# Performance work log

Hardware: AMD Instinct MI355X
Metric: run time of the kernel (lower is better)

The kernel has to match this reference:

```python
import jax, jax.numpy as jnp
import numpy as np

IMG_H, IMG_W = 800, 800
OUT_H, OUT_W = 7, 7
SR = 2  # sampling_ratio (exact sampling branch)
SCALES = (0.25, 0.125, 0.0625, 0.03125)
CANONICAL_SCALE = 224.0
CANONICAL_LEVEL = 4.0
K_MIN, K_MAX = 2, 5  # -log2(0.25), -log2(1/32)
EPS = 1e-6


def _prep_coords(c, size):
    # c: continuous coords (K, N); returns low/high int indices and lerp weights
    c = jnp.maximum(c, 0.0)
    lo = c.astype(jnp.int32)  # truncation == floor for c >= 0
    at_edge = lo >= size - 1
    hi = jnp.where(at_edge, size - 1, lo + 1)
    lo = jnp.where(at_edge, size - 1, lo)
    l = c - lo.astype(c.dtype)
    return lo, hi, l, 1.0 - l


def roi_align_exact(feat, batch_idx, rois, scale):
    # feat: (B, C, H, W); batch_idx: (K,) int; rois: (K, 4) xyxy; exact sampling, aligned=False
    B, C, H, W = feat.shape
    x1 = rois[:, 0] * scale
    y1 = rois[:, 1] * scale
    x2 = rois[:, 2] * scale
    y2 = rois[:, 3] * scale
    roi_w = jnp.maximum(x2 - x1, 1.0)
    roi_h = jnp.maximum(y2 - y1, 1.0)
    bin_h = roi_h / OUT_H
    bin_w = roi_w / OUT_W
    ph = jnp.arange(OUT_H, dtype=feat.dtype)
    pw = jnp.arange(OUT_W, dtype=feat.dtype)
    iy = jnp.arange(SR, dtype=feat.dtype)
    ix = jnp.arange(SR, dtype=feat.dtype)
    # (K, OUT_H, SR) -> (K, OUT_H*SR)
    y = y1[:, None, None] + ph[None, :, None] * bin_h[:, None, None] + (iy[None, None, :] + 0.5) * (bin_h / SR)[:, None, None]
    x = x1[:, None, None] + pw[None, :, None] * bin_w[:, None, None] + (ix[None, None, :] + 0.5) * (bin_w / SR)[:, None, None]
    K = rois.shape[0]
    NY, NX = OUT_H * SR, OUT_W * SR
    y = y.reshape(K, NY)
    x = x.reshape(K, NX)
    y_lo, y_hi, ly, hy = _prep_coords(y, H)
    x_lo, x_hi, lx, hx = _prep_coords(x, W)

    b = batch_idx[:, None, None]

    def gather(yi, xi):
        # -> (K, NY, NX, C): advanced indices around ':' put (K,NY,NX) in front
        return feat[b, :, yi[:, :, None], xi[:, None, :]]

    val = (hy[:, :, None, None] * hx[:, None, :, None] * gather(y_lo, x_lo)
           + hy[:, :, None, None] * lx[:, None, :, None] * gather(y_lo, x_hi)
           + ly[:, :, None, None] * hx[:, None, :, None] * gather(y_hi, x_lo)
           + ly[:, :, None, None] * lx[:, None, :, None] * gather(y_hi, x_hi))
    # (K, OUT_H, SR, OUT_W, SR, C) -> sum sampling grid, avg by count
    val = val.reshape(K, OUT_H, SR, OUT_W, SR, C).sum(axis=(2, 4)) / float(SR * SR)
    return jnp.transpose(val, (0, 3, 1, 2))  # (K, C, OUT_H, OUT_W)


def multiscale_roi_align(feats, boxes):
    B, L, _ = boxes.shape
    K = B * L
    rois = boxes.reshape(K, 4)
    batch_idx = jnp.repeat(jnp.arange(B, dtype=jnp.int32), L)
    area = (rois[:, 2] - rois[:, 0]) * (rois[:, 3] - rois[:, 1])
    s = jnp.sqrt(area)
    lvl = jnp.floor(CANONICAL_LEVEL + jnp.log2(s / CANONICAL_SCALE) + EPS)
    levels = jnp.clip(lvl, K_MIN, K_MAX).astype(jnp.int32) - K_MIN
    C = feats[0].shape[1]
    out = jnp.zeros((K, C, OUT_H, OUT_W), dtype=feats[0].dtype)
    for l, (f, sc) in enumerate(zip(feats, SCALES)):
        pooled = roi_align_exact(f, batch_idx, rois, sc)
        out = out + jnp.where((levels == l)[:, None, None, None], pooled, 0.0)
    return out


def setup_inputs() -> dict:
    key = jax.random.key(0)
    k0, k1, k2, k3, kw, kh, kx, ky = jax.random.split(key, 8)
    B, C, L = 2, 256, 256
    feat0 = jax.random.normal(k0, (B, C, 200, 200), dtype=jnp.float32)
    feat1 = jax.random.normal(k1, (B, C, 100, 100), dtype=jnp.float32)
    feat2 = jax.random.normal(k2, (B, C, 50, 50), dtype=jnp.float32)
    feat3 = jax.random.normal(k3, (B, C, 25, 25), dtype=jnp.float32)
    w = jax.random.uniform(kw, (B, L), minval=16.0, maxval=512.0)
    h = jax.random.uniform(kh, (B, L), minval=16.0, maxval=512.0)
    x1 = jax.random.uniform(kx, (B, L)) * (IMG_W - w)
    y1 = jax.random.uniform(ky, (B, L)) * (IMG_H - h)
    boxes = jnp.stack([x1, y1, x1 + w, y1 + h], axis=-1).astype(jnp.float32)
    return {"feat0": feat0, "feat1": feat1, "feat2": feat2, "feat3": feat3, "boxes": boxes}


def reference(feat0, feat1, feat2, feat3, boxes):
    return multiscale_roi_align([feat0, feat1, feat2, feat3], boxes)
```

## Files before the change

kernel.cpp:

```cpp
#include <hip/hip_runtime.h>


#define OUT_HW 7
#define NCH 256
#define CC 8
#define PM 1152
#define WSTRIDE 80
#define NROI 512
#define THREADS 512


__device__ __forceinline__ void roi_scalars(const float* __restrict__ boxes, int k,
    int& lvl, int& H, int& W, float& x1, float& y1, float& bin_w, float& bin_h,
    int& px0, int& py0, int& pw_cnt, int& ph_cnt)
{
    float bx1 = boxes[k*4+0], by1 = boxes[k*4+1], bx2 = boxes[k*4+2], by2 = boxes[k*4+3];
    float area = (bx2-bx1)*(by2-by1);
    float s = sqrtf(area);
    float lvlf = floorf(4.0f + log2f(s*(1.0f/224.0f)) + 1e-6f);
    lvlf = fminf(fmaxf(lvlf, 2.0f), 5.0f);
    lvl = (int)lvlf - 2;
    float scale;
    if (lvl == 0)      { H=200; W=200; scale=0.25f;    }
    else if (lvl == 1) { H=100; W=100; scale=0.125f;   }
    else if (lvl == 2) { H=50;  W=50;  scale=0.0625f;  }
    else               { H=25;  W=25;  scale=0.03125f; }
    x1 = bx1*scale; y1 = by1*scale;
    float roi_w = fmaxf(bx2*scale - x1, 1.0f);
    float roi_h = fmaxf(by2*scale - y1, 1.0f);
    bin_w = roi_w*(1.0f/7.0f); bin_h = roi_h*(1.0f/7.0f);
    float c; int lo;
    c = fmaxf(x1 + 0.25f*bin_w, 0.0f); lo = (int)c; px0 = (lo >= W-1) ? (W-1) : lo;
    c = fmaxf(x1 + 6.75f*bin_w, 0.0f); lo = (int)c; int px1e = (lo >= W-1) ? (W-1) : (lo+1);
    c = fmaxf(y1 + 0.25f*bin_h, 0.0f); lo = (int)c; py0 = (lo >= H-1) ? (H-1) : lo;
    c = fmaxf(y1 + 6.75f*bin_h, 0.0f); lo = (int)c; int py1e = (lo >= H-1) ? (H-1) : (lo+1);
    pw_cnt = px1e - px0 + 1;
    ph_cnt = py1e - py0 + 1;
}

__global__ __launch_bounds__(64) void roi_setup(const float* __restrict__ boxes,
                                                int* __restrict__ ws)
{
    int k = blockIdx.x*64 + threadIdx.x;
    if (k >= NROI) return;
    int lvl, H, W, px0, py0, pw_cnt, ph_cnt;
    float x1, y1, bin_w, bin_h;
    roi_scalars(boxes, k, lvl, H, W, x1, y1, bin_w, bin_h, px0, py0, pw_cnt, ph_cnt);
    int pw_pad = (pw_cnt + 1) | 1;
    int* p = ws + k*WSTRIDE;
    p[0]=lvl; p[1]=px0; p[2]=py0; p[3]=pw_cnt; p[4]=pw_pad;
    p[5]=pw_cnt*ph_cnt; p[6]=W; p[7]=H*W; p[8]=ph_cnt;
    for (int i = 0; i < 14; ++i) {
        float c = fmaxf(x1 + ((float)i*0.5f + 0.25f)*bin_w, 0.0f);
        int lo = (int)c; int xle; float lx;
        if (lo >= W-1) { xle = (W-1) - px0; lx = 0.0f; }
        else           { xle = lo - px0;    lx = c - (float)lo; }
        p[16+i] = xle;
        p[30+i] = __float_as_int(lx);
    }
    for (int i = 0; i < 14; ++i) {
        float c = fmaxf(y1 + ((float)i*0.5f + 0.25f)*bin_h, 0.0f);
        int lo = (int)c; int r; float ly;
        if (lo >= H-1) { r = (H-1) - py0; ly = 0.0f; }
        else           { r = lo - py0;    ly = c - (float)lo; }
        p[44+i] = r*pw_pad;
        p[58+i] = __float_as_int(ly);
    }
}

template<bool USE_WS>
__global__ __launch_bounds__(THREADS) void msroi_main(
    const float* __restrict__ f0, const float* __restrict__ f1,
    const float* __restrict__ f2, const float* __restrict__ f3,
    const float* __restrict__ boxes, const int* __restrict__ ws,
    float* __restrict__ out)
{
    __shared__ float s_patch[CC*PM];
    __shared__ int   s_taps[56];

    const int tid = threadIdx.x;
    const int k  = blockIdx.y;
    const int c0 = blockIdx.x * CC;

    int lvl, px0, py0, pw_cnt, pw_pad, pdense, W, HW, ph_cnt;
    if constexpr (USE_WS) {
        const int* p = ws + k*WSTRIDE;
        lvl = p[0]; px0 = p[1]; py0 = p[2]; pw_cnt = p[3]; pw_pad = p[4];
        pdense = p[5]; W = p[6]; HW = p[7]; ph_cnt = p[8];
        if (tid < 56) s_taps[tid] = p[16 + tid];
    } else {
        int H; float x1, y1, bin_w, bin_h;
        roi_scalars(boxes, k, lvl, H, W, x1, y1, bin_w, bin_h, px0, py0, pw_cnt, ph_cnt);
        pw_pad = (pw_cnt + 1) | 1; pdense = pw_cnt*ph_cnt; HW = H*W;
        if (tid < 14) {
            float c = fmaxf(x1 + ((float)tid*0.5f + 0.25f)*bin_w, 0.0f);
            int lo = (int)c; int xle; float lx;
            if (lo >= W-1) { xle = (W-1) - px0; lx = 0.0f; }
            else           { xle = lo - px0;    lx = c - (float)lo; }
            s_taps[tid] = xle; s_taps[14+tid] = __float_as_int(lx);
        } else if (tid >= 64 && tid < 78) {
            int i = tid - 64;
            float c = fmaxf(y1 + ((float)i*0.5f + 0.25f)*bin_h, 0.0f);
            int lo = (int)c; int r; float ly;
            if (lo >= H-1) { r = (H-1) - py0; ly = 0.0f; }
            else           { r = lo - py0;    ly = c - (float)lo; }
            s_taps[28+i] = r*pw_pad; s_taps[42+i] = __float_as_int(ly);
        }
    }

    const float* feat = (lvl == 0) ? f0 : (lvl == 1) ? f1 : (lvl == 2) ? f2 : f3;
    const int b = k >> 8;
    const float* bp = feat + (size_t)(b*NCH + c0) * (size_t)HW;

    int nz = ph_cnt + 1 + pw_cnt;
    for (int z = tid; z < nz; z += THREADS) {
        int wi = (z <= ph_cnt) ? (z*pw_pad + pw_cnt)
                               : (ph_cnt*pw_pad + (z - (ph_cnt + 1)));
#pragma unroll
        for (int j = 0; j < CC; ++j) s_patch[j*PM + wi] = 0.0f;
    }

    float inv_pw = 1.0f / (float)pw_cnt;
    for (int i = tid; i < pdense; i += THREADS) {
        int r = (int)((float)i * inv_pw);
        int col = i - r*pw_cnt;
        if (col < 0)             { col += pw_cnt; --r; }
        else if (col >= pw_cnt)  { col -= pw_cnt; ++r; }
        int go = (py0 + r)*W + (px0 + col);
        int wi = r*pw_pad + col;
#pragma unroll
        for (int j = 0; j < CC; ++j)
            s_patch[j*PM + wi] = bp[(size_t)j*(size_t)HW + (size_t)go];
    }
    __syncthreads();

    if (tid < CC*49) {
        int cl = tid / 49, pix = tid - cl*49;
        int ph = pix / 7,  pw  = pix - ph*7;
        int cb = cl*PM;
        int xl0 = s_taps[2*pw]   + cb;
        int xl1 = s_taps[2*pw+1] + cb;
        float lx0 = __int_as_float(s_taps[14 + 2*pw]);
        float lx1 = __int_as_float(s_taps[15 + 2*pw]);
        int r00 = s_taps[28 + 2*ph];
        int r01 = s_taps[29 + 2*ph];
        float ly0 = __int_as_float(s_taps[42 + 2*ph]);
        float ly1 = __int_as_float(s_taps[43 + 2*ph]);
        float hx0 = 1.0f - lx0, hx1 = 1.0f - lx1;
        float hy0 = 1.0f - ly0, hy1 = 1.0f - ly1;

        float acc = 0.0f;
        {
            int a = r00 + xl0, a2 = a + pw_pad;
            float v00 = s_patch[a], v01 = s_patch[a+1];
            float v10 = s_patch[a2], v11 = s_patch[a2+1];
            acc += hy0*(hx0*v00 + lx0*v01) + ly0*(hx0*v10 + lx0*v11);
        }
        {
            int a = r00 + xl1, a2 = a + pw_pad;
            float v00 = s_patch[a], v01 = s_patch[a+1];
            float v10 = s_patch[a2], v11 = s_patch[a2+1];
            acc += hy0*(hx1*v00 + lx1*v01) + ly0*(hx1*v10 + lx1*v11);
        }
        {
            int a = r01 + xl0, a2 = a + pw_pad;
            float v00 = s_patch[a], v01 = s_patch[a+1];
            float v10 = s_patch[a2], v11 = s_patch[a2+1];
            acc += hy1*(hx0*v00 + lx0*v01) + ly1*(hx0*v10 + lx0*v11);
        }
        {
            int a = r01 + xl1, a2 = a + pw_pad;
            float v00 = s_patch[a], v01 = s_patch[a+1];
            float v10 = s_patch[a2], v11 = s_patch[a2+1];
            acc += hy1*(hx1*v00 + lx1*v01) + ly1*(hx1*v10 + lx1*v11);
        }
        out[((size_t)k*NCH + c0)*49 + tid] = acc * 0.25f;
    }
}

extern "C" void kernel_launch(void* const* d_in, const int* in_sizes, int n_in,
                              void* d_out, int out_size, void* d_ws, size_t ws_size,
                              hipStream_t stream)
{
    const float* f0 = (const float*)d_in[0];
    const float* f1 = (const float*)d_in[1];
    const float* f2 = (const float*)d_in[2];
    const float* f3 = (const float*)d_in[3];
    const float* boxes = (const float*)d_in[4];
    float* out = (float*)d_out;

    dim3 grid(NCH / CC, NROI, 1);
    dim3 block(THREADS, 1, 1);
    size_t need = (size_t)NROI * WSTRIDE * sizeof(int);

    if (d_ws != nullptr && ws_size >= need) {
        roi_setup<<<dim3((NROI + 63)/64), dim3(64), 0, stream>>>(boxes, (int*)d_ws);
        msroi_main<true><<<grid, block, 0, stream>>>(f0, f1, f2, f3, boxes,
                                                     (const int*)d_ws, out);
    } else {
        msroi_main<false><<<grid, block, 0, stream>>>(f0, f1, f2, f3, boxes,
                                                      nullptr, out);
    }
}
```

Baseline: 176.9 us.

## Double-buffer channel chunks via direct global-to-LDS loads per block

Each block now processes 64 channels in 8 chunks of 8. It double-buffers the staged patch in LDS, loading the next chunk with global_load_lds while the current one is interpolated. The padded patch layout is replaced by a dense pw_cnt stride with a zeroed tail, and tap offsets are read once into registers. This cuts grid size and per-block setup and overlaps load with compute, but it lowers the number of blocks and so the parallelism, and it depends on async-copy wait semantics.

```diff
diff --git a/kernel.cpp b/kernel.cpp
--- a/kernel.cpp
+++ b/kernel.cpp
@@ -1,13 +1,18 @@
 #include <hip/hip_runtime.h>
 
 
-#define OUT_HW 7
 #define NCH 256
 #define CC 8
-#define PM 1152
+#define CHUNKS 8
+#define CPB (CC * CHUNKS)
+#define PM 1153
 #define WSTRIDE 80
 #define NROI 512
 #define THREADS 512
+#define NPIX (CC * 49)
+
+typedef const __attribute__((address_space(1))) void* gas_ptr;
+typedef __attribute__((address_space(3))) void* las_ptr;
 
 
 __device__ __forceinline__ void roi_scalars(const float* __restrict__ boxes, int k,
@@ -46,10 +51,10 @@
     int lvl, H, W, px0, py0, pw_cnt, ph_cnt;
     float x1, y1, bin_w, bin_h;
     roi_scalars(boxes, k, lvl, H, W, x1, y1, bin_w, bin_h, px0, py0, pw_cnt, ph_cnt);
-    int pw_pad = (pw_cnt + 1) | 1;
+    int pdense = pw_cnt * ph_cnt;
     int* p = ws + k*WSTRIDE;
-    p[0]=lvl; p[1]=px0; p[2]=py0; p[3]=pw_cnt; p[4]=pw_pad;
-    p[5]=pw_cnt*ph_cnt; p[6]=W; p[7]=H*W; p[8]=ph_cnt;
+    p[0]=lvl; p[1]=px0; p[2]=py0; p[3]=pw_cnt; p[4]=pdense; p[5]=W; p[6]=H*W;
+    p[7]=(pdense + THREADS - 1)/THREADS;
     for (int i = 0; i < 14; ++i) {
         float c = fmaxf(x1 + ((float)i*0.5f + 0.25f)*bin_w, 0.0f);
         int lo = (int)c; int xle; float lx;
@@ -63,118 +68,141 @@
         int lo = (int)c; int r; float ly;
         if (lo >= H-1) { r = (H-1) - py0; ly = 0.0f; }
         else           { r = lo - py0;    ly = c - (float)lo; }
-        p[44+i] = r*pw_pad;
+        p[44+i] = r*pw_cnt;
         p[58+i] = __float_as_int(ly);
     }
 }
 
 template<bool USE_WS>
-__global__ __launch_bounds__(THREADS) void msroi_main(
+__global__ __launch_bounds__(THREADS) void msroi_pipe(
     const float* __restrict__ f0, const float* __restrict__ f1,
     const float* __restrict__ f2, const float* __restrict__ f3,
     const float* __restrict__ boxes, const int* __restrict__ ws,
     float* __restrict__ out)
 {
-    __shared__ float s_patch[CC*PM];
-    __shared__ int   s_taps[56];
+    __shared__ float s_patch[2][CC * PM];
 
     const int tid = threadIdx.x;
     const int k  = blockIdx.y;
-    const int c0 = blockIdx.x * CC;
-
-    int lvl, px0, py0, pw_cnt, pw_pad, pdense, W, HW, ph_cnt;
+    const int c0 = blockIdx.x * CPB;
+
+    int lvl, px0, py0, pw_cnt, pdense, W, HW, nit;
+    int Hf = 0; float x1f = 0, y1f = 0, bwf = 0, bhf = 0;
     if constexpr (USE_WS) {
         const int* p = ws + k*WSTRIDE;
-        lvl = p[0]; px0 = p[1]; py0 = p[2]; pw_cnt = p[3]; pw_pad = p[4];
-        pdense = p[5]; W = p[6]; HW = p[7]; ph_cnt = p[8];
-        if (tid < 56) s_taps[tid] = p[16 + tid];
+        lvl = p[0]; px0 = p[1]; py0 = p[2]; pw_cnt = p[3];
+        pdense = p[4]; W = p[5]; HW = p[6]; nit = p[7];
     } else {
-        int H; float x1, y1, bin_w, bin_h;
-        roi_scalars(boxes, k, lvl, H, W, x1, y1, bin_w, bin_h, px0, py0, pw_cnt, ph_cnt);
-        pw_pad = (pw_cnt + 1) | 1; pdense = pw_cnt*ph_cnt; HW = H*W;
-        if (tid < 14) {
-            float c = fmaxf(x1 + ((float)tid*0.5f + 0.25f)*bin_w, 0.0f);
-            int lo = (int)c; int xle; float lx;
-            if (lo >= W-1) { xle = (W-1) - px0; lx = 0.0f; }
-            else           { xle = lo - px0;    lx = c - (float)lo; }
-            s_taps[tid] = xle; s_taps[14+tid] = __float_as_int(lx);
-        } else if (tid >= 64 && tid < 78) {
-            int i = tid - 64;
-            float c = fmaxf(y1 + ((float)i*0.5f + 0.25f)*bin_h, 0.0f);
-            int lo = (int)c; int r; float ly;
-            if (lo >= H-1) { r = (H-1) - py0; ly = 0.0f; }
-            else           { r = lo - py0;    ly = c - (float)lo; }
-            s_taps[28+i] = r*pw_pad; s_taps[42+i] = __float_as_int(ly);
-        }
+        int ph_cnt;
+        roi_scalars(boxes, k, lvl, Hf, W, x1f, y1f, bwf, bhf, px0, py0, pw_cnt, ph_cnt);
+        pdense = pw_cnt * ph_cnt; HW = Hf * W;
+        nit = (pdense + THREADS - 1)/THREADS;
     }
 
     const float* feat = (lvl == 0) ? f0 : (lvl == 1) ? f1 : (lvl == 2) ? f2 : f3;
     const int b = k >> 8;
     const float* bp = feat + (size_t)(b*NCH + c0) * (size_t)HW;
 
-    int nz = ph_cnt + 1 + pw_cnt;
-    for (int z = tid; z < nz; z += THREADS) {
-        int wi = (z <= ph_cnt) ? (z*pw_pad + pw_cnt)
-                               : (ph_cnt*pw_pad + (z - (ph_cnt + 1)));
-#pragma unroll
-        for (int j = 0; j < CC; ++j) s_patch[j*PM + wi] = 0.0f;
-    }
-
-    float inv_pw = 1.0f / (float)pw_cnt;
-    for (int i = tid; i < pdense; i += THREADS) {
-        int r = (int)((float)i * inv_pw);
-        int col = i - r*pw_cnt;
-        if (col < 0)             { col += pw_cnt; --r; }
-        else if (col >= pw_cnt)  { col -= pw_cnt; ++r; }
-        int go = (py0 + r)*W + (px0 + col);
-        int wi = r*pw_pad + col;
-#pragma unroll
-        for (int j = 0; j < CC; ++j)
-            s_patch[j*PM + wi] = bp[(size_t)j*(size_t)HW + (size_t)go];
-    }
-    __syncthreads();
-
-    if (tid < CC*49) {
+    int aR0C0 = 0, aR0C1 = 0, aR1C0 = 0, aR1C1 = 0, clbase = 0;
+    float lx0 = 0, lx1 = 0, ly0 = 0, ly1 = 0, hx0 = 0, hx1 = 0, hy0 = 0, hy1 = 0;
+    if (tid < NPIX) {
         int cl = tid / 49, pix = tid - cl*49;
         int ph = pix / 7,  pw  = pix - ph*7;
-        int cb = cl*PM;
-        int xl0 = s_taps[2*pw]   + cb;
-        int xl1 = s_taps[2*pw+1] + cb;
-        float lx0 = __int_as_float(s_taps[14 + 2*pw]);
-        float lx1 = __int_as_float(s_taps[15 + 2*pw]);
-        int r00 = s_taps[28 + 2*ph];
-        int r01 = s_taps[29 + 2*ph];
-        float ly0 = __int_as_float(s_taps[42 + 2*ph]);
-        float ly1 = __int_as_float(s_taps[43 + 2*ph]);
-        float hx0 = 1.0f - lx0, hx1 = 1.0f - lx1;
-        float hy0 = 1.0f - ly0, hy1 = 1.0f - ly1;
-
-        float acc = 0.0f;
-        {
-            int a = r00 + xl0, a2 = a + pw_pad;
-            float v00 = s_patch[a], v01 = s_patch[a+1];
-            float v10 = s_patch[a2], v11 = s_patch[a2+1];
-            acc += hy0*(hx0*v00 + lx0*v01) + ly0*(hx0*v10 + lx0*v11);
-        }
-        {
-            int a = r00 + xl1, a2 = a + pw_pad;
-            float v00 = s_patch[a], v01 = s_patch[a+1];
-            float v10 = s_patch[a2], v11 = s_patch[a2+1];
-            acc += hy0*(hx1*v00 + lx1*v01) + ly0*(hx1*v10 + lx1*v11);
-        }
-        {
-            int a = r01 + xl0, a2 = a + pw_pad;
-            float v00 = s_patch[a], v01 = s_patch[a+1];
-            float v10 = s_patch[a2], v11 = s_patch[a2+1];
-            acc += hy1*(hx0*v00 + lx0*v01) + ly1*(hx0*v10 + lx0*v11);
-        }
-        {
-            int a = r01 + xl1, a2 = a + pw_pad;
-            float v00 = s_patch[a], v01 = s_patch[a+1];
-            float v10 = s_patch[a2], v11 = s_patch[a2+1];
-            acc += hy1*(hx1*v00 + lx1*v01) + ly1*(hx1*v10 + lx1*v11);
-        }
-        out[((size_t)k*NCH + c0)*49 + tid] = acc * 0.25f;
+        clbase = cl * PM;
+        int xe0, xe1, r00, r01;
+        if constexpr (USE_WS) {
+            const int* p = ws + k*WSTRIDE;
+            xe0 = p[16 + 2*pw]; xe1 = p[17 + 2*pw];
+            lx0 = __int_as_float(p[30 + 2*pw]); lx1 = __int_as_float(p[31 + 2*pw]);
+            r00 = p[44 + 2*ph]; r01 = p[45 + 2*ph];
+            ly0 = __int_as_float(p[58 + 2*ph]); ly1 = __int_as_float(p[59 + 2*ph]);
+        } else {
+            auto tapx = [&](int i, int& xe, float& lx) {
+                float c = fmaxf(x1f + ((float)i*0.5f + 0.25f)*bwf, 0.0f);
+                int lo = (int)c;
+                if (lo >= W-1) { xe = (W-1) - px0; lx = 0.0f; }
+                else           { xe = lo - px0;    lx = c - (float)lo; }
+            };
+            auto tapy = [&](int i, int& r0, float& ly) {
+                float c = fmaxf(y1f + ((float)i*0.5f + 0.25f)*bhf, 0.0f);
+                int lo = (int)c;
+                if (lo >= Hf-1) { r0 = ((Hf-1) - py0)*pw_cnt; ly = 0.0f; }
+                else            { r0 = (lo - py0)*pw_cnt;     ly = c - (float)lo; }
+            };
+            tapx(2*pw, xe0, lx0); tapx(2*pw+1, xe1, lx1);
+            tapy(2*ph, r00, ly0); tapy(2*ph+1, r01, ly1);
+        }
+        aR0C0 = r00 + xe0; aR0C1 = r00 + xe1;
+        aR1C0 = r01 + xe0; aR1C1 = r01 + xe1;
+        hx0 = 1.0f - lx0; hx1 = 1.0f - lx1;
+        hy0 = 1.0f - ly0; hy1 = 1.0f - ly1;
+    }
+
+    {
+        int glen = PM - pdense; if (glen > 123) glen = 123;
+        int tot = 2 * CC * glen;
+        for (int z = tid; z < tot; z += THREADS) {
+            int bufc = z / glen, off = z - bufc*glen;
+            s_patch[bufc >> 3][(bufc & 7)*PM + pdense + off] = 0.0f;
+        }
+    }
+
+    const float inv_pw = 1.0f / (float)pw_cnt;
+    const int pstr = pw_cnt;
+
+    auto stage = [&](int chunk, int buf) {
+        const float* cbp = bp + (size_t)(chunk * CC) * (size_t)HW;
+        for (int it = 0; it < nit; ++it) {
+            int i = it*THREADS + tid;
+            int gi = (i < pdense) ? i : (pdense - 1);
+            int r = (int)((float)gi * inv_pw);
+            int col = gi - r*pw_cnt;
+            if (col < 0)             { col += pw_cnt; --r; }
+            else if (col >= pw_cnt)  { col -= pw_cnt; ++r; }
+            int go = (py0 + r)*W + (px0 + col);
+            const float* src = cbp + go;
+            float* dst = &s_patch[buf][i];
+#pragma unroll
+            for (int j = 0; j < CC; ++j) {
+                __builtin_amdgcn_global_load_lds((gas_ptr)(src + (size_t)j*HW),
+                                                 (las_ptr)(dst + j*PM), 4, 0, 0);
+            }
+        }
+    };
+
+    __syncthreads();
+    int cur = 0;
+    stage(0, 0);
+    asm volatile("s_waitcnt vmcnt(0)" ::: "memory");
+    __syncthreads();
+
+    const size_t obase = ((size_t)k*NCH + c0)*49 + tid;
+    for (int n = 0; n < CHUNKS; ++n) {
+        if (n + 1 < CHUNKS) stage(n + 1, cur ^ 1);
+        if (tid < NPIX) {
+            const float* patch = &s_patch[cur][clbase];
+            float acc;
+            {   int a = aR0C0;
+                float v00 = patch[a], v01 = patch[a+1];
+                float v10 = patch[a+pstr], v11 = patch[a+pstr+1];
+                acc  = hy0*(hx0*v00 + lx0*v01) + ly0*(hx0*v10 + lx0*v11); }
+            {   int a = aR0C1;
+                float v00 = patch[a], v01 = patch[a+1];
+                float v10 = patch[a+pstr], v11 = patch[a+pstr+1];
+                acc += hy0*(hx1*v00 + lx1*v01) + ly0*(hx1*v10 + lx1*v11); }
+            {   int a = aR1C0;
+                float v00 = patch[a], v01 = patch[a+1];
+                float v10 = patch[a+pstr], v11 = patch[a+pstr+1];
+                acc += hy1*(hx0*v00 + lx0*v01) + ly1*(hx0*v10 + lx0*v11); }
+            {   int a = aR1C1;
+                float v00 = patch[a], v01 = patch[a+1];
+                float v10 = patch[a+pstr], v11 = patch[a+pstr+1];
+                acc += hy1*(hx1*v00 + lx1*v01) + ly1*(hx1*v10 + lx1*v11); }
+            out[obase + (size_t)n * NPIX] = acc * 0.25f;
+        }
+        asm volatile("s_waitcnt vmcnt(0)" ::: "memory");
+        __syncthreads();
+        cur ^= 1;
     }
 }
 
@@ -189,16 +217,16 @@
     const float* boxes = (const float*)d_in[4];
     float* out = (float*)d_out;
 
-    dim3 grid(NCH / CC, NROI, 1);
+    dim3 grid(NCH / CPB, NROI, 1);
     dim3 block(THREADS, 1, 1);
     size_t need = (size_t)NROI * WSTRIDE * sizeof(int);
 
     if (d_ws != nullptr && ws_size >= need) {
         roi_setup<<<dim3((NROI + 63)/64), dim3(64), 0, stream>>>(boxes, (int*)d_ws);
-        msroi_main<true><<<grid, block, 0, stream>>>(f0, f1, f2, f3, boxes,
+        msroi_pipe<true><<<grid, block, 0, stream>>>(f0, f1, f2, f3, boxes,
                                                      (const int*)d_ws, out);
     } else {
-        msroi_main<false><<<grid, block, 0, stream>>>(f0, f1, f2, f3, boxes,
+        msroi_pipe<false><<<grid, block, 0, stream>>>(f0, f1, f2, f3, boxes,
                                                       nullptr, out);
     }
 }
```

New measurement: 194.1 us. 9.7% more time.
